# Kernel tuning notes

Hardware: AMD Instinct MI355X
Metric: run time of the kernel (lower is better)

Reference implementation:

```python
import jax, jax.numpy as jnp
import numpy as np

EMBED = 32
HEADS = 8
HEAD_DIM = EMBED // HEADS  # 4


def setup_inputs() -> dict:
    key = jax.random.key(0)
    ks = jax.random.split(key, 12)
    N, Q, K = 4, 2048, 2048
    inp = {
        "query": jax.random.normal(ks[0], (N, Q, EMBED), dtype=jnp.float32),
        "key": jax.random.normal(ks[1], (N, K, EMBED), dtype=jnp.float32),
        "value": jax.random.normal(ks[2], (N, K, EMBED), dtype=jnp.float32),
        "mask": jnp.ones((N, 1, Q, K), dtype=jnp.int32),
        # nn.Linear params: W stored as (in, out) here; math y = x @ W + b
        "Wq": jax.random.normal(ks[3], (EMBED, EMBED), dtype=jnp.float32) / np.sqrt(EMBED),
        "bq": jax.random.normal(ks[4], (EMBED,), dtype=jnp.float32) * 0.01,
        "Wk": jax.random.normal(ks[5], (EMBED, EMBED), dtype=jnp.float32) / np.sqrt(EMBED),
        "bk": jax.random.normal(ks[6], (EMBED,), dtype=jnp.float32) * 0.01,
        "Wv": jax.random.normal(ks[7], (EMBED, EMBED), dtype=jnp.float32) / np.sqrt(EMBED),
        "bv": jax.random.normal(ks[8], (EMBED,), dtype=jnp.float32) * 0.01,
        "Wo": jax.random.normal(ks[9], (EMBED, EMBED), dtype=jnp.float32) / np.sqrt(EMBED),
        "bo": jax.random.normal(ks[10], (EMBED,), dtype=jnp.float32) * 0.01,
    }
    return inp


def reference(query, key, value, mask, Wq, bq, Wk, bk, Wv, bv, Wo, bo):
    N, Qlen, _ = query.shape
    Klen = key.shape[1]
    # linear projections
    q = (query @ Wq + bq).reshape(N, Qlen, HEADS, HEAD_DIM)
    k = (key @ Wk + bk).reshape(N, Klen, HEADS, HEAD_DIM)
    v = (value @ Wv + bv).reshape(N, Klen, HEADS, HEAD_DIM)
    # energy: [N, H, Q, K]
    energy = jnp.einsum("nqhd,nkhd->nhqk", q, k)
    energy = jnp.where(mask == 0, jnp.float32(-1e20), energy)
    # NOTE: original scales by sqrt(embedSize), not sqrt(headDim)
    attn = jax.nn.softmax(energy / jnp.sqrt(jnp.float32(EMBED)), axis=3)
    out = jnp.einsum("nhqv,nvhd->nqhd", attn, v).reshape(N, Qlen, EMBED)
    return out @ Wo + bo
```

## Files before the change

kernel.cpp:

```cpp
#include <hip/hip_runtime.h>

#define NB 4
#define SEQ 2048
#define EMB 32
#define HEADS 8
#define HD 4

typedef float v2f __attribute__((ext_vector_type(2)));
typedef unsigned int uint;

__device__ __forceinline__ v2f splat2(float x) { v2f r; r.x = x; r.y = x; return r; }
__device__ __forceinline__ v2f pkfma(v2f a, v2f b, v2f c) {
  return __builtin_elementwise_fma(a, b, c);
}

__global__ __launch_bounds__(256) void pack_proj_kernel(
    const int* __restrict__ mask, uint* __restrict__ pmw,
    const float* __restrict__ key, const float* __restrict__ value,
    const float* __restrict__ Wk, const float* __restrict__ bk,
    const float* __restrict__ Wv, const float* __restrict__ bv,
    float* __restrict__ Kp, float* __restrict__ Vp) {
  const int packBlocks = NB * SEQ * SEQ / 4 / 256;
  if (blockIdx.x < packBlocks) {
    int g = blockIdx.x * 256 + threadIdx.x;
    const int4 v = ((const int4*)mask)[g];
    uint nib = (uint)(v.x != 0) | ((uint)(v.y != 0) << 1) |
               ((uint)(v.z != 0) << 2) | ((uint)(v.w != 0) << 3);
    int lane = threadIdx.x & 63;
    uint w = nib << (4 * (lane & 7));
    w |= __shfl_xor(w, 1);
    w |= __shfl_xor(w, 2);
    w |= __shfl_xor(w, 4);
    if ((lane & 7) == 0) pmw[g >> 3] = w;
  } else {
    const int half = NB * SEQ / 8;
    int blk2 = blockIdx.x - packBlocks;
    bool isV = blk2 >= half;
    const float* X = isV ? value : key;
    const float* W = isV ? Wv : Wk;
    const float* b = isV ? bv : bk;
    float* P = isV ? Vp : Kp;
    int blk = isV ? (blk2 - half) : blk2;

    __shared__ float sW[EMB][EMB];
    __shared__ float sb[EMB];
    __shared__ float sX[8][EMB];
    int t = threadIdx.x;
    for (int i = t; i < EMB * EMB; i += 256) sW[i >> 5][i & 31] = W[i];
    if (t < EMB) sb[t] = b[t];
    size_t row0 = (size_t)blk * 8;
    int r = t >> 5, c = t & 31;
    sX[r][c] = X[(row0 + r) * EMB + c];
    __syncthreads();
    float acc = sb[c];
#pragma unroll
    for (int d = 0; d < EMB; ++d) acc = fmaf(sX[r][d], sW[d][c], acc);
    P[(row0 + r) * EMB + c] = acc;
  }
}

__device__ __forceinline__ void load_tile(
    const float*& kptr, const float*& vptr,
    float4 (&KK)[4], float4 (&VV)[4]) {
  KK[0] = *(const float4*)(kptr);
  KK[1] = *(const float4*)(kptr + EMB);
  KK[2] = *(const float4*)(kptr + 2 * EMB);
  KK[3] = *(const float4*)(kptr + 3 * EMB);
  VV[0] = *(const float4*)(vptr);
  VV[1] = *(const float4*)(vptr + EMB);
  VV[2] = *(const float4*)(vptr + 2 * EMB);
  VV[3] = *(const float4*)(vptr + 3 * EMB);
  kptr += 32 * EMB; vptr += 32 * EMB;
}

__device__ __forceinline__ void compute_tile(
    const float4 (&KK)[4], const float4 (&VV)[4],
    const v2f (&q2)[4][4], v2f (&l2)[4], v2f (&ac2)[4][4]) {
#pragma unroll
  for (int p = 0; p < 4; ++p) {
    v2f pf[4];
#pragma unroll
    for (int j = 0; j < 4; ++j) {
      const float4 kk = KK[j];
      v2f s = pkfma(q2[p][0], splat2(kk.x),
              pkfma(q2[p][1], splat2(kk.y),
              pkfma(q2[p][2], splat2(kk.z), q2[p][3] * splat2(kk.w))));
      pf[j].x = __builtin_amdgcn_exp2f(s.x);
      pf[j].y = __builtin_amdgcn_exp2f(s.y);
    }
    l2[p] += (pf[0] + pf[1]) + (pf[2] + pf[3]);
#pragma unroll
    for (int j = 0; j < 4; ++j) {
      const float4 vv = VV[j];
      ac2[p][0] = pkfma(pf[j], splat2(vv.x), ac2[p][0]);
      ac2[p][1] = pkfma(pf[j], splat2(vv.y), ac2[p][1]);
      ac2[p][2] = pkfma(pf[j], splat2(vv.z), ac2[p][2]);
      ac2[p][3] = pkfma(pf[j], splat2(vv.w), ac2[p][3]);
    }
  }
}

__device__ __forceinline__ void compute_tile_masked(
    const float4 (&KK)[4], const float4 (&VV)[4],
    const uint (&MW)[8], int ks4,
    const v2f (&q2)[4][4], v2f (&l2)[4], v2f (&ac2)[4][4]) {
#pragma unroll
  for (int p = 0; p < 4; ++p) {
    v2f pf[4];
#pragma unroll
    for (int j = 0; j < 4; ++j) {
      const float4 kk = KK[j];
      v2f s = pkfma(q2[p][0], splat2(kk.x),
              pkfma(q2[p][1], splat2(kk.y),
              pkfma(q2[p][2], splat2(kk.z), q2[p][3] * splat2(kk.w))));
      pf[j].x = ((MW[2 * p + 0] >> (ks4 + j)) & 1u) ? __builtin_amdgcn_exp2f(s.x) : 0.0f;
      pf[j].y = ((MW[2 * p + 1] >> (ks4 + j)) & 1u) ? __builtin_amdgcn_exp2f(s.y) : 0.0f;
    }
    l2[p] += (pf[0] + pf[1]) + (pf[2] + pf[3]);
#pragma unroll
    for (int j = 0; j < 4; ++j) {
      const float4 vv = VV[j];
      ac2[p][0] = pkfma(pf[j], splat2(vv.x), ac2[p][0]);
      ac2[p][1] = pkfma(pf[j], splat2(vv.y), ac2[p][1]);
      ac2[p][2] = pkfma(pf[j], splat2(vv.z), ac2[p][2]);
      ac2[p][3] = pkfma(pf[j], splat2(vv.w), ac2[p][3]);
    }
  }
}

__global__ __launch_bounds__(256, 2) void attn_kernel(
    const float* __restrict__ query, const uint* __restrict__ pmw,
    const float* __restrict__ Kp, const float* __restrict__ Vp,
    const float* __restrict__ Wq, const float* __restrict__ bq,
    const float* __restrict__ Wo, const float* __restrict__ bo,
    float* __restrict__ out) {
  __shared__ float sWq[EMB][EMB];
  __shared__ float sWo[EMB][EMB];
  __shared__ float sbq[EMB];
  __shared__ float sbo[EMB];
  __shared__ float sX[16][EMB];
  __shared__ float sCtx[16][EMB + 1];
  __shared__ float sPart[2][16][EMB];
  __shared__ float sL[2][16][HEADS];

  int t = threadIdx.x;
  int n = blockIdx.x >> 7;
  int qt = blockIdx.x & 127;
  int qrow0 = qt * 16;

  int w = t >> 6;
  int octet = w >> 1;
  int kh = w & 1;
  int lane = t & 63;
  int h = lane & 7;
  int ks = lane >> 3;
  int ks4 = 4 * ks;
  int rbl = 8 * octet;

  for (int i = t; i < EMB * EMB; i += 256) {
    sWq[i >> 5][i & 31] = Wq[i];
    sWo[i >> 5][i & 31] = Wo[i];
  }
  if (t < EMB) { sbq[t] = bq[t]; sbo[t] = bo[t]; }
#pragma unroll
  for (int rr = 0; rr < 2; ++rr) {
    int r = (t >> 5) + 8 * rr, c = t & 31;
    sX[r][c] = query[((size_t)n * SEQ + qrow0 + r) * EMB + c];
  }
  __syncthreads();

  const float SC = 0.17677669529663687f * 1.4426950408889634f;
  v2f q2[4][4];
#pragma unroll
  for (int p = 0; p < 4; ++p)
#pragma unroll
    for (int d = 0; d < 4; ++d) q2[p][d] = splat2(sbq[4 * h + d]);
#pragma unroll
  for (int j = 0; j < EMB; ++j) {
    float w0 = sWq[j][4 * h + 0], w1 = sWq[j][4 * h + 1];
    float w2 = sWq[j][4 * h + 2], w3 = sWq[j][4 * h + 3];
#pragma unroll
    for (int p = 0; p < 4; ++p) {
      v2f x;
      x.x = sX[rbl + 2 * p + 0][j];
      x.y = sX[rbl + 2 * p + 1][j];
      q2[p][0] = pkfma(x, splat2(w0), q2[p][0]);
      q2[p][1] = pkfma(x, splat2(w1), q2[p][1]);
      q2[p][2] = pkfma(x, splat2(w2), q2[p][2]);
      q2[p][3] = pkfma(x, splat2(w3), q2[p][3]);
    }
  }
#pragma unroll
  for (int p = 0; p < 4; ++p)
#pragma unroll
    for (int d = 0; d < 4; ++d) q2[p][d] *= splat2(SC);

  const uint* mbase = pmw + ((size_t)n * SEQ + qrow0 + rbl) * (SEQ / 32) + kh * 32;
  int wl = lane & 7, rl = lane >> 3;
  const uint* mr = mbase + (size_t)rl * 64;
  uint myand = mr[wl] & mr[wl + 8] & mr[wl + 16] & mr[wl + 24];
  bool allones = __all(myand == 0xFFFFFFFFu);

  const float* kptr = Kp + (size_t)n * SEQ * EMB + (size_t)kh * 1024 * EMB
                         + (size_t)ks4 * EMB + 4 * h;
  const float* vptr = Vp + (size_t)n * SEQ * EMB + (size_t)kh * 1024 * EMB
                         + (size_t)ks4 * EMB + 4 * h;

  v2f l2[4], ac2[4][4];
#pragma unroll
  for (int p = 0; p < 4; ++p) {
    l2[p] = splat2(0.0f);
#pragma unroll
    for (int d = 0; d < 4; ++d) ac2[p][d] = splat2(0.0f);
  }

  if (allones) {
    float4 ka[4], va[4], kb[4], vb[4];
    load_tile(kptr, vptr, ka, va);
    for (int i = 0; i < 15; ++i) {
      load_tile(kptr, vptr, kb, vb);
      compute_tile(ka, va, q2, l2, ac2);
      load_tile(kptr, vptr, ka, va);
      compute_tile(kb, vb, q2, l2, ac2);
    }
    load_tile(kptr, vptr, kb, vb);
    compute_tile(ka, va, q2, l2, ac2);
    compute_tile(kb, vb, q2, l2, ac2);
  } else {
    for (int tile = 0; tile < 32; ++tile) {
      float4 ka[4], va[4];
      load_tile(kptr, vptr, ka, va);
      uint MW[8];
#pragma unroll
      for (int rr = 0; rr < 8; ++rr) MW[rr] = mbase[(size_t)rr * 64 + tile];
      compute_tile_masked(ka, va, MW, ks4, q2, l2, ac2);
    }
  }

#pragma unroll
  for (int d = 8; d <= 32; d <<= 1) {
#pragma unroll
    for (int p = 0; p < 4; ++p) {
      l2[p].x += __shfl_xor(l2[p].x, d);
      l2[p].y += __shfl_xor(l2[p].y, d);
#pragma unroll
      for (int e = 0; e < 4; ++e) {
        ac2[p][e].x += __shfl_xor(ac2[p][e].x, d);
        ac2[p][e].y += __shfl_xor(ac2[p][e].y, d);
      }
    }
  }

#pragma unroll
  for (int p = 0; p < 4; ++p) {
    int r0 = rbl + 2 * p;
    if (ks < 4) {
      float vA = (ks == 0) ? ac2[p][0].x : (ks == 1) ? ac2[p][1].x
               : (ks == 2) ? ac2[p][2].x : ac2[p][3].x;
      float vB = (ks == 0) ? ac2[p][0].y : (ks == 1) ? ac2[p][1].y
               : (ks == 2) ? ac2[p][2].y : ac2[p][3].y;
      sPart[kh][r0 + 0][4 * h + ks] = vA;
      sPart[kh][r0 + 1][4 * h + ks] = vB;
    } else if (ks == 4) {
      sL[kh][r0 + 0][h] = l2[p].x;
      sL[kh][r0 + 1][h] = l2[p].y;
    }
  }
  __syncthreads();

#pragma unroll
  for (int rr = 0; rr < 2; ++rr) {
    int r = (t >> 5) + 8 * rr, c = t & 31, hh = (t & 31) >> 2;
    float num = sPart[0][r][c] + sPart[1][r][c];
    float den = sL[0][r][hh] + sL[1][r][hh];
    sCtx[r][c] = num * __builtin_amdgcn_rcpf(den);
  }
  __syncthreads();

#pragma unroll
  for (int rr = 0; rr < 2; ++rr) {
    int r = (t >> 5) + 8 * rr, e = t & 31;
    float o = sbo[e];
#pragma unroll
    for (int j = 0; j < EMB; ++j) o = fmaf(sCtx[r][j], sWo[j][e], o);
    out[((size_t)n * SEQ + qrow0 + r) * EMB + e] = o;
  }
}

extern "C" void kernel_launch(void* const* d_in, const int* in_sizes, int n_in,
                              void* d_out, int out_size, void* d_ws, size_t ws_size,
                              hipStream_t stream) {
  const float* query = (const float*)d_in[0];
  const float* key   = (const float*)d_in[1];
  const float* value = (const float*)d_in[2];
  const int*   mask  = (const int*)d_in[3];
  const float* Wq = (const float*)d_in[4];
  const float* bq = (const float*)d_in[5];
  const float* Wk = (const float*)d_in[6];
  const float* bk = (const float*)d_in[7];
  const float* Wv = (const float*)d_in[8];
  const float* bv = (const float*)d_in[9];
  const float* Wo = (const float*)d_in[10];
  const float* bo = (const float*)d_in[11];
  float* out = (float*)d_out;

  float* Kp = (float*)d_ws;
  float* Vp = Kp + (size_t)NB * SEQ * EMB;
  uint* pmw = (uint*)(Vp + (size_t)NB * SEQ * EMB);

  const int packBlocks = NB * SEQ * SEQ / 4 / 256;
  const int projBlocks = 2 * NB * SEQ / 8;
  pack_proj_kernel<<<dim3(packBlocks + projBlocks), dim3(256), 0, stream>>>(
      mask, pmw, key, value, Wk, bk, Wv, bv, Kp, Vp);
  attn_kernel<<<dim3(NB * (SEQ / 16)), dim3(256), 0, stream>>>(
      query, pmw, Kp, Vp, Wq, bq, Wo, bo, out);
}
```

Measured before the change: 58.98 us.

## Split attention blocks into 8 query rows with four-way key split

The attention kernel now handles 8 query rows per block instead of 16, and its four wavefronts each cover a quarter of the keys (512) instead of two row-groups times two key halves. The grid doubles to 1024 blocks and partial sums are combined across four key quarters in shared memory. This is meant to raise parallelism and shorten each wave's serial loop, at the cost of loading the Wq/Wo weights twice as often across blocks and repeating the Q projection. The launch-bounds occupancy hint is also dropped.

```diff
diff --git a/kernel.cpp b/kernel.cpp
--- a/kernel.cpp
+++ b/kernel.cpp
@@ -128,7 +128,7 @@
   }
 }
 
-__global__ __launch_bounds__(256, 2) void attn_kernel(
+__global__ __launch_bounds__(256) void attn_kernel(
     const float* __restrict__ query, const uint* __restrict__ pmw,
     const float* __restrict__ Kp, const float* __restrict__ Vp,
     const float* __restrict__ Wq, const float* __restrict__ bq,
@@ -138,33 +138,29 @@
   __shared__ float sWo[EMB][EMB];
   __shared__ float sbq[EMB];
   __shared__ float sbo[EMB];
-  __shared__ float sX[16][EMB];
-  __shared__ float sCtx[16][EMB + 1];
-  __shared__ float sPart[2][16][EMB];
-  __shared__ float sL[2][16][HEADS];
+  __shared__ float sX[8][EMB];
+  __shared__ float sCtx[8][EMB + 1];
+  __shared__ float sPart[4][8][EMB];
+  __shared__ float sL[4][8][HEADS];
 
   int t = threadIdx.x;
-  int n = blockIdx.x >> 7;
-  int qt = blockIdx.x & 127;
-  int qrow0 = qt * 16;
-
-  int w = t >> 6;
-  int octet = w >> 1;
-  int kh = w & 1;
+  int n = blockIdx.x >> 8;
+  int qt = blockIdx.x & 255;
+  int qrow0 = qt * 8;
+
+  int kq = t >> 6;
   int lane = t & 63;
   int h = lane & 7;
   int ks = lane >> 3;
   int ks4 = 4 * ks;
-  int rbl = 8 * octet;
 
   for (int i = t; i < EMB * EMB; i += 256) {
     sWq[i >> 5][i & 31] = Wq[i];
     sWo[i >> 5][i & 31] = Wo[i];
   }
   if (t < EMB) { sbq[t] = bq[t]; sbo[t] = bo[t]; }
-#pragma unroll
-  for (int rr = 0; rr < 2; ++rr) {
-    int r = (t >> 5) + 8 * rr, c = t & 31;
+  {
+    int r = t >> 5, c = t & 31;
     sX[r][c] = query[((size_t)n * SEQ + qrow0 + r) * EMB + c];
   }
   __syncthreads();
@@ -177,17 +173,19 @@
     for (int d = 0; d < 4; ++d) q2[p][d] = splat2(sbq[4 * h + d]);
 #pragma unroll
   for (int j = 0; j < EMB; ++j) {
-    float w0 = sWq[j][4 * h + 0], w1 = sWq[j][4 * h + 1];
-    float w2 = sWq[j][4 * h + 2], w3 = sWq[j][4 * h + 3];
+    v2f w0 = splat2(sWq[j][4 * h + 0]);
+    v2f w1 = splat2(sWq[j][4 * h + 1]);
+    v2f w2 = splat2(sWq[j][4 * h + 2]);
+    v2f w3 = splat2(sWq[j][4 * h + 3]);
 #pragma unroll
     for (int p = 0; p < 4; ++p) {
       v2f x;
-      x.x = sX[rbl + 2 * p + 0][j];
-      x.y = sX[rbl + 2 * p + 1][j];
-      q2[p][0] = pkfma(x, splat2(w0), q2[p][0]);
-      q2[p][1] = pkfma(x, splat2(w1), q2[p][1]);
-      q2[p][2] = pkfma(x, splat2(w2), q2[p][2]);
-      q2[p][3] = pkfma(x, splat2(w3), q2[p][3]);
+      x.x = sX[2 * p + 0][j];
+      x.y = sX[2 * p + 1][j];
+      q2[p][0] = pkfma(x, w0, q2[p][0]);
+      q2[p][1] = pkfma(x, w1, q2[p][1]);
+      q2[p][2] = pkfma(x, w2, q2[p][2]);
+      q2[p][3] = pkfma(x, w3, q2[p][3]);
     }
   }
 #pragma unroll
@@ -195,15 +193,15 @@
 #pragma unroll
     for (int d = 0; d < 4; ++d) q2[p][d] *= splat2(SC);
 
-  const uint* mbase = pmw + ((size_t)n * SEQ + qrow0 + rbl) * (SEQ / 32) + kh * 32;
+  const uint* mbase = pmw + ((size_t)n * SEQ + qrow0) * (SEQ / 32) + kq * 16;
   int wl = lane & 7, rl = lane >> 3;
   const uint* mr = mbase + (size_t)rl * 64;
-  uint myand = mr[wl] & mr[wl + 8] & mr[wl + 16] & mr[wl + 24];
+  uint myand = mr[wl] & mr[wl + 8];
   bool allones = __all(myand == 0xFFFFFFFFu);
 
-  const float* kptr = Kp + (size_t)n * SEQ * EMB + (size_t)kh * 1024 * EMB
+  const float* kptr = Kp + (size_t)n * SEQ * EMB + (size_t)kq * 512 * EMB
                          + (size_t)ks4 * EMB + 4 * h;
-  const float* vptr = Vp + (size_t)n * SEQ * EMB + (size_t)kh * 1024 * EMB
+  const float* vptr = Vp + (size_t)n * SEQ * EMB + (size_t)kq * 512 * EMB
                          + (size_t)ks4 * EMB + 4 * h;
 
   v2f l2[4], ac2[4][4];
@@ -217,7 +215,7 @@
   if (allones) {
     float4 ka[4], va[4], kb[4], vb[4];
     load_tile(kptr, vptr, ka, va);
-    for (int i = 0; i < 15; ++i) {
+    for (int i = 0; i < 7; ++i) {
       load_tile(kptr, vptr, kb, vb);
       compute_tile(ka, va, q2, l2, ac2);
       load_tile(kptr, vptr, ka, va);
@@ -227,7 +225,7 @@
     compute_tile(ka, va, q2, l2, ac2);
     compute_tile(kb, vb, q2, l2, ac2);
   } else {
-    for (int tile = 0; tile < 32; ++tile) {
+    for (int tile = 0; tile < 16; ++tile) {
       float4 ka[4], va[4];
       load_tile(kptr, vptr, ka, va);
       uint MW[8];
@@ -253,33 +251,32 @@
 
 #pragma unroll
   for (int p = 0; p < 4; ++p) {
-    int r0 = rbl + 2 * p;
+    int r0 = 2 * p;
     if (ks < 4) {
       float vA = (ks == 0) ? ac2[p][0].x : (ks == 1) ? ac2[p][1].x
                : (ks == 2) ? ac2[p][2].x : ac2[p][3].x;
       float vB = (ks == 0) ? ac2[p][0].y : (ks == 1) ? ac2[p][1].y
                : (ks == 2) ? ac2[p][2].y : ac2[p][3].y;
-      sPart[kh][r0 + 0][4 * h + ks] = vA;
-      sPart[kh][r0 + 1][4 * h + ks] = vB;
+      sPart[kq][r0 + 0][4 * h + ks] = vA;
+      sPart[kq][r0 + 1][4 * h + ks] = vB;
     } else if (ks == 4) {
-      sL[kh][r0 + 0][h] = l2[p].x;
-      sL[kh][r0 + 1][h] = l2[p].y;
+      sL[kq][r0 + 0][h] = l2[p].x;
+      sL[kq][r0 + 1][h] = l2[p].y;
     }
   }
   __syncthreads();
 
-#pragma unroll
-  for (int rr = 0; rr < 2; ++rr) {
-    int r = (t >> 5) + 8 * rr, c = t & 31, hh = (t & 31) >> 2;
-    float num = sPart[0][r][c] + sPart[1][r][c];
-    float den = sL[0][r][hh] + sL[1][r][hh];
+  {
+    int r = t >> 5, c = t & 31, hh = (t & 31) >> 2;
+    float num = (sPart[0][r][c] + sPart[1][r][c]) +
+                (sPart[2][r][c] + sPart[3][r][c]);
+    float den = (sL[0][r][hh] + sL[1][r][hh]) + (sL[2][r][hh] + sL[3][r][hh]);
     sCtx[r][c] = num * __builtin_amdgcn_rcpf(den);
   }
   __syncthreads();
 
-#pragma unroll
-  for (int rr = 0; rr < 2; ++rr) {
-    int r = (t >> 5) + 8 * rr, e = t & 31;
+  {
+    int r = t >> 5, e = t & 31;
     float o = sbo[e];
 #pragma unroll
     for (int j = 0; j < EMB; ++j) o = fmaf(sCtx[r][j], sWo[j][e], o);
@@ -312,6 +309,6 @@
   const int projBlocks = 2 * NB * SEQ / 8;
   pack_proj_kernel<<<dim3(packBlocks + projBlocks), dim3(256), 0, stream>>>(
       mask, pmw, key, value, Wk, bk, Wv, bv, Kp, Vp);
-  attn_kernel<<<dim3(NB * (SEQ / 16)), dim3(256), 0, stream>>>(
+  attn_kernel<<<dim3(NB * (SEQ / 8)), dim3(256), 0, stream>>>(
       query, pmw, Kp, Vp, Wq, bq, Wo, bo, out);
 }
```

New measurement: 65.49 us. 1.11x slower.

## Drop mask bit-packing pass; read int mask directly in attention kernel

Applied to the files above, without the earlier changes.

Removes the separate mask-packing stage and has the attention kernel read the raw int32 mask directly. It checks for an all-ones tile by AND-reducing int4 loads and uses the mask values per element on the masked path. This avoids writing and re-reading a packed bitmask, and the first kernel becomes a pure K/V projection. The inner loops also switch from packed v2f FMAs to scalar FMAs over 8 rows per thread, and the occupancy hint in launch_bounds is removed. The full mask is still read once, now inside attention, and scalar math may issue more instructions than the packed version.

```diff
diff --git a/kernel.cpp b/kernel.cpp
--- a/kernel.cpp
+++ b/kernel.cpp
@@ -6,57 +6,35 @@
 #define HEADS 8
 #define HD 4
 
-typedef float v2f __attribute__((ext_vector_type(2)));
 typedef unsigned int uint;
 
-__device__ __forceinline__ v2f splat2(float x) { v2f r; r.x = x; r.y = x; return r; }
-__device__ __forceinline__ v2f pkfma(v2f a, v2f b, v2f c) {
-  return __builtin_elementwise_fma(a, b, c);
-}
-
-__global__ __launch_bounds__(256) void pack_proj_kernel(
-    const int* __restrict__ mask, uint* __restrict__ pmw,
+__global__ __launch_bounds__(256) void proj_kv_kernel(
     const float* __restrict__ key, const float* __restrict__ value,
     const float* __restrict__ Wk, const float* __restrict__ bk,
     const float* __restrict__ Wv, const float* __restrict__ bv,
     float* __restrict__ Kp, float* __restrict__ Vp) {
-  const int packBlocks = NB * SEQ * SEQ / 4 / 256;
-  if (blockIdx.x < packBlocks) {
-    int g = blockIdx.x * 256 + threadIdx.x;
-    const int4 v = ((const int4*)mask)[g];
-    uint nib = (uint)(v.x != 0) | ((uint)(v.y != 0) << 1) |
-               ((uint)(v.z != 0) << 2) | ((uint)(v.w != 0) << 3);
-    int lane = threadIdx.x & 63;
-    uint w = nib << (4 * (lane & 7));
-    w |= __shfl_xor(w, 1);
-    w |= __shfl_xor(w, 2);
-    w |= __shfl_xor(w, 4);
-    if ((lane & 7) == 0) pmw[g >> 3] = w;
-  } else {
-    const int half = NB * SEQ / 8;
-    int blk2 = blockIdx.x - packBlocks;
-    bool isV = blk2 >= half;
-    const float* X = isV ? value : key;
-    const float* W = isV ? Wv : Wk;
-    const float* b = isV ? bv : bk;
-    float* P = isV ? Vp : Kp;
-    int blk = isV ? (blk2 - half) : blk2;
-
-    __shared__ float sW[EMB][EMB];
-    __shared__ float sb[EMB];
-    __shared__ float sX[8][EMB];
-    int t = threadIdx.x;
-    for (int i = t; i < EMB * EMB; i += 256) sW[i >> 5][i & 31] = W[i];
-    if (t < EMB) sb[t] = b[t];
-    size_t row0 = (size_t)blk * 8;
-    int r = t >> 5, c = t & 31;
-    sX[r][c] = X[(row0 + r) * EMB + c];
-    __syncthreads();
-    float acc = sb[c];
-#pragma unroll
-    for (int d = 0; d < EMB; ++d) acc = fmaf(sX[r][d], sW[d][c], acc);
-    P[(row0 + r) * EMB + c] = acc;
-  }
+  const int half = NB * SEQ / 8;
+  bool isV = blockIdx.x >= half;
+  const float* X = isV ? value : key;
+  const float* W = isV ? Wv : Wk;
+  const float* b = isV ? bv : bk;
+  float* P = isV ? Vp : Kp;
+  int blk = isV ? (blockIdx.x - half) : blockIdx.x;
+
+  __shared__ float sW[EMB][EMB];
+  __shared__ float sb[EMB];
+  __shared__ float sX[8][EMB];
+  int t = threadIdx.x;
+  for (int i = t; i < EMB * EMB; i += 256) sW[i >> 5][i & 31] = W[i];
+  if (t < EMB) sb[t] = b[t];
+  size_t row0 = (size_t)blk * 8;
+  int r = t >> 5, c = t & 31;
+  sX[r][c] = X[(row0 + r) * EMB + c];
+  __syncthreads();
+  float acc = sb[c];
+#pragma unroll
+  for (int d = 0; d < EMB; ++d) acc = fmaf(sX[r][d], sW[d][c], acc);
+  P[(row0 + r) * EMB + c] = acc;
 }
 
 __device__ __forceinline__ void load_tile(
@@ -75,61 +53,49 @@
 
 __device__ __forceinline__ void compute_tile(
     const float4 (&KK)[4], const float4 (&VV)[4],
-    const v2f (&q2)[4][4], v2f (&l2)[4], v2f (&ac2)[4][4]) {
-#pragma unroll
-  for (int p = 0; p < 4; ++p) {
-    v2f pf[4];
-#pragma unroll
-    for (int j = 0; j < 4; ++j) {
-      const float4 kk = KK[j];
-      v2f s = pkfma(q2[p][0], splat2(kk.x),
-              pkfma(q2[p][1], splat2(kk.y),
-              pkfma(q2[p][2], splat2(kk.z), q2[p][3] * splat2(kk.w))));
-      pf[j].x = __builtin_amdgcn_exp2f(s.x);
-      pf[j].y = __builtin_amdgcn_exp2f(s.y);
-    }
-    l2[p] += (pf[0] + pf[1]) + (pf[2] + pf[3]);
-#pragma unroll
-    for (int j = 0; j < 4; ++j) {
-      const float4 vv = VV[j];
-      ac2[p][0] = pkfma(pf[j], splat2(vv.x), ac2[p][0]);
-      ac2[p][1] = pkfma(pf[j], splat2(vv.y), ac2[p][1]);
-      ac2[p][2] = pkfma(pf[j], splat2(vv.z), ac2[p][2]);
-      ac2[p][3] = pkfma(pf[j], splat2(vv.w), ac2[p][3]);
+    const float (&q)[8][4], float (&l)[8], float (&ac)[8][4]) {
+#pragma unroll
+  for (int j = 0; j < 4; ++j) {
+    const float4 kk = KK[j];
+    const float4 vv = VV[j];
+#pragma unroll
+    for (int r = 0; r < 8; ++r) {
+      float s = fmaf(q[r][0], kk.x, fmaf(q[r][1], kk.y,
+                fmaf(q[r][2], kk.z, q[r][3] * kk.w)));
+      float p = __builtin_amdgcn_exp2f(s);
+      l[r] += p;
+      ac[r][0] = fmaf(p, vv.x, ac[r][0]);
+      ac[r][1] = fmaf(p, vv.y, ac[r][1]);
+      ac[r][2] = fmaf(p, vv.z, ac[r][2]);
+      ac[r][3] = fmaf(p, vv.w, ac[r][3]);
     }
   }
 }
 
 __device__ __forceinline__ void compute_tile_masked(
-    const float4 (&KK)[4], const float4 (&VV)[4],
-    const uint (&MW)[8], int ks4,
-    const v2f (&q2)[4][4], v2f (&l2)[4], v2f (&ac2)[4][4]) {
-#pragma unroll
-  for (int p = 0; p < 4; ++p) {
-    v2f pf[4];
-#pragma unroll
-    for (int j = 0; j < 4; ++j) {
-      const float4 kk = KK[j];
-      v2f s = pkfma(q2[p][0], splat2(kk.x),
-              pkfma(q2[p][1], splat2(kk.y),
-              pkfma(q2[p][2], splat2(kk.z), q2[p][3] * splat2(kk.w))));
-      pf[j].x = ((MW[2 * p + 0] >> (ks4 + j)) & 1u) ? __builtin_amdgcn_exp2f(s.x) : 0.0f;
-      pf[j].y = ((MW[2 * p + 1] >> (ks4 + j)) & 1u) ? __builtin_amdgcn_exp2f(s.y) : 0.0f;
-    }
-    l2[p] += (pf[0] + pf[1]) + (pf[2] + pf[3]);
-#pragma unroll
-    for (int j = 0; j < 4; ++j) {
-      const float4 vv = VV[j];
-      ac2[p][0] = pkfma(pf[j], splat2(vv.x), ac2[p][0]);
-      ac2[p][1] = pkfma(pf[j], splat2(vv.y), ac2[p][1]);
-      ac2[p][2] = pkfma(pf[j], splat2(vv.z), ac2[p][2]);
-      ac2[p][3] = pkfma(pf[j], splat2(vv.w), ac2[p][3]);
-    }
-  }
-}
-
-__global__ __launch_bounds__(256, 2) void attn_kernel(
-    const float* __restrict__ query, const uint* __restrict__ pmw,
+    const float4 (&KK)[4], const float4 (&VV)[4], const int4 (&MQ)[8],
+    const float (&q)[8][4], float (&l)[8], float (&ac)[8][4]) {
+#pragma unroll
+  for (int j = 0; j < 4; ++j) {
+    const float4 kk = KK[j];
+    const float4 vv = VV[j];
+#pragma unroll
+    for (int r = 0; r < 8; ++r) {
+      float s = fmaf(q[r][0], kk.x, fmaf(q[r][1], kk.y,
+                fmaf(q[r][2], kk.z, q[r][3] * kk.w)));
+      int m = (j == 0) ? MQ[r].x : (j == 1) ? MQ[r].y : (j == 2) ? MQ[r].z : MQ[r].w;
+      float p = m ? __builtin_amdgcn_exp2f(s) : 0.0f;
+      l[r] += p;
+      ac[r][0] = fmaf(p, vv.x, ac[r][0]);
+      ac[r][1] = fmaf(p, vv.y, ac[r][1]);
+      ac[r][2] = fmaf(p, vv.z, ac[r][2]);
+      ac[r][3] = fmaf(p, vv.w, ac[r][3]);
+    }
+  }
+}
+
+__global__ __launch_bounds__(256) void attn_kernel(
+    const float* __restrict__ query, const int* __restrict__ mask,
     const float* __restrict__ Kp, const float* __restrict__ Vp,
     const float* __restrict__ Wq, const float* __restrict__ bq,
     const float* __restrict__ Wo, const float* __restrict__ bo,
@@ -170,48 +136,53 @@
   __syncthreads();
 
   const float SC = 0.17677669529663687f * 1.4426950408889634f;
-  v2f q2[4][4];
-#pragma unroll
-  for (int p = 0; p < 4; ++p)
-#pragma unroll
-    for (int d = 0; d < 4; ++d) q2[p][d] = splat2(sbq[4 * h + d]);
+  float q[8][4];
+#pragma unroll
+  for (int r = 0; r < 8; ++r)
+#pragma unroll
+    for (int d = 0; d < 4; ++d) q[r][d] = sbq[4 * h + d];
 #pragma unroll
   for (int j = 0; j < EMB; ++j) {
     float w0 = sWq[j][4 * h + 0], w1 = sWq[j][4 * h + 1];
     float w2 = sWq[j][4 * h + 2], w3 = sWq[j][4 * h + 3];
 #pragma unroll
-    for (int p = 0; p < 4; ++p) {
-      v2f x;
-      x.x = sX[rbl + 2 * p + 0][j];
-      x.y = sX[rbl + 2 * p + 1][j];
-      q2[p][0] = pkfma(x, splat2(w0), q2[p][0]);
-      q2[p][1] = pkfma(x, splat2(w1), q2[p][1]);
-      q2[p][2] = pkfma(x, splat2(w2), q2[p][2]);
-      q2[p][3] = pkfma(x, splat2(w3), q2[p][3]);
-    }
-  }
-#pragma unroll
-  for (int p = 0; p < 4; ++p)
-#pragma unroll
-    for (int d = 0; d < 4; ++d) q2[p][d] *= splat2(SC);
-
-  const uint* mbase = pmw + ((size_t)n * SEQ + qrow0 + rbl) * (SEQ / 32) + kh * 32;
-  int wl = lane & 7, rl = lane >> 3;
-  const uint* mr = mbase + (size_t)rl * 64;
-  uint myand = mr[wl] & mr[wl + 8] & mr[wl + 16] & mr[wl + 24];
-  bool allones = __all(myand == 0xFFFFFFFFu);
+    for (int r = 0; r < 8; ++r) {
+      float x = sX[rbl + r][j];
+      q[r][0] = fmaf(x, w0, q[r][0]);
+      q[r][1] = fmaf(x, w1, q[r][1]);
+      q[r][2] = fmaf(x, w2, q[r][2]);
+      q[r][3] = fmaf(x, w3, q[r][3]);
+    }
+  }
+#pragma unroll
+  for (int r = 0; r < 8; ++r)
+#pragma unroll
+    for (int d = 0; d < 4; ++d) q[r][d] *= SC;
+
+  const int* msl = mask + ((size_t)n * SEQ + qrow0 + rbl) * SEQ + kh * 1024;
+  uint andv = 0xFFFFFFFFu;
+#pragma unroll
+  for (int rr = 0; rr < 8; ++rr) {
+    const int4* mrow = (const int4*)(msl + (size_t)rr * SEQ);
+#pragma unroll
+    for (int c = 0; c < 4; ++c) {
+      int4 v = mrow[64 * c + lane];
+      andv &= (uint)v.x & (uint)v.y & (uint)v.z & (uint)v.w;
+    }
+  }
+  bool allones = __all(andv == 0xFFFFFFFFu);
 
   const float* kptr = Kp + (size_t)n * SEQ * EMB + (size_t)kh * 1024 * EMB
                          + (size_t)ks4 * EMB + 4 * h;
   const float* vptr = Vp + (size_t)n * SEQ * EMB + (size_t)kh * 1024 * EMB
                          + (size_t)ks4 * EMB + 4 * h;
 
-  v2f l2[4], ac2[4][4];
-#pragma unroll
-  for (int p = 0; p < 4; ++p) {
-    l2[p] = splat2(0.0f);
-#pragma unroll
-    for (int d = 0; d < 4; ++d) ac2[p][d] = splat2(0.0f);
+  float l[8], ac[8][4];
+#pragma unroll
+  for (int r = 0; r < 8; ++r) {
+    l[r] = 0.0f;
+#pragma unroll
+    for (int d = 0; d < 4; ++d) ac[r][d] = 0.0f;
   }
 
   if (allones) {
@@ -219,52 +190,45 @@
     load_tile(kptr, vptr, ka, va);
     for (int i = 0; i < 15; ++i) {
       load_tile(kptr, vptr, kb, vb);
-      compute_tile(ka, va, q2, l2, ac2);
+      compute_tile(ka, va, q, l, ac);
       load_tile(kptr, vptr, ka, va);
-      compute_tile(kb, vb, q2, l2, ac2);
+      compute_tile(kb, vb, q, l, ac);
     }
     load_tile(kptr, vptr, kb, vb);
-    compute_tile(ka, va, q2, l2, ac2);
-    compute_tile(kb, vb, q2, l2, ac2);
+    compute_tile(ka, va, q, l, ac);
+    compute_tile(kb, vb, q, l, ac);
   } else {
     for (int tile = 0; tile < 32; ++tile) {
       float4 ka[4], va[4];
       load_tile(kptr, vptr, ka, va);
-      uint MW[8];
-#pragma unroll
-      for (int rr = 0; rr < 8; ++rr) MW[rr] = mbase[(size_t)rr * 64 + tile];
-      compute_tile_masked(ka, va, MW, ks4, q2, l2, ac2);
+      int4 MQ[8];
+#pragma unroll
+      for (int rr = 0; rr < 8; ++rr)
+        MQ[rr] = *(const int4*)(msl + (size_t)rr * SEQ + tile * 32 + ks4);
+      compute_tile_masked(ka, va, MQ, q, l, ac);
     }
   }
 
 #pragma unroll
   for (int d = 8; d <= 32; d <<= 1) {
 #pragma unroll
-    for (int p = 0; p < 4; ++p) {
-      l2[p].x += __shfl_xor(l2[p].x, d);
-      l2[p].y += __shfl_xor(l2[p].y, d);
-#pragma unroll
-      for (int e = 0; e < 4; ++e) {
-        ac2[p][e].x += __shfl_xor(ac2[p][e].x, d);
-        ac2[p][e].y += __shfl_xor(ac2[p][e].y, d);
-      }
-    }
-  }
-
-#pragma unroll
-  for (int p = 0; p < 4; ++p) {
-    int r0 = rbl + 2 * p;
-    if (ks < 4) {
-      float vA = (ks == 0) ? ac2[p][0].x : (ks == 1) ? ac2[p][1].x
-               : (ks == 2) ? ac2[p][2].x : ac2[p][3].x;
-      float vB = (ks == 0) ? ac2[p][0].y : (ks == 1) ? ac2[p][1].y
-               : (ks == 2) ? ac2[p][2].y : ac2[p][3].y;
-      sPart[kh][r0 + 0][4 * h + ks] = vA;
-      sPart[kh][r0 + 1][4 * h + ks] = vB;
-    } else if (ks == 4) {
-      sL[kh][r0 + 0][h] = l2[p].x;
-      sL[kh][r0 + 1][h] = l2[p].y;
-    }
+    for (int r = 0; r < 8; ++r) {
+      l[r] += __shfl_xor(l[r], d);
+#pragma unroll
+      for (int e = 0; e < 4; ++e) ac[r][e] += __shfl_xor(ac[r][e], d);
+    }
+  }
+
+  if (ks < 4) {
+#pragma unroll
+    for (int r = 0; r < 8; ++r) {
+      float v = (ks == 0) ? ac[r][0] : (ks == 1) ? ac[r][1]
+              : (ks == 2) ? ac[r][2] : ac[r][3];
+      sPart[kh][rbl + r][4 * h + ks] = v;
+    }
+  } else if (ks == 4) {
+#pragma unroll
+    for (int r = 0; r < 8; ++r) sL[kh][rbl + r][h] = l[r];
   }
   __syncthreads();
 
@@ -306,12 +270,9 @@
 
   float* Kp = (float*)d_ws;
   float* Vp = Kp + (size_t)NB * SEQ * EMB;
-  uint* pmw = (uint*)(Vp + (size_t)NB * SEQ * EMB);
-
-  const int packBlocks = NB * SEQ * SEQ / 4 / 256;
-  const int projBlocks = 2 * NB * SEQ / 8;
-  pack_proj_kernel<<<dim3(packBlocks + projBlocks), dim3(256), 0, stream>>>(
-      mask, pmw, key, value, Wk, bk, Wv, bv, Kp, Vp);
+
+  proj_kv_kernel<<<dim3(2 * NB * SEQ / 8), dim3(256), 0, stream>>>(
+      key, value, Wk, bk, Wv, bv, Kp, Vp);
   attn_kernel<<<dim3(NB * (SEQ / 16)), dim3(256), 0, stream>>>(
-      query, pmw, Kp, Vp, Wq, bq, Wo, bo, out);
-}
+      query, mask, Kp, Vp, Wq, bq, Wo, bo, out);
+}
```

Result: slower. 71.66 us (+21.5%).

## Stage K/V tiles through LDS with async global_load_lds triple buffering

Applied to the files above, without the earlier changes.

In the all-ones mask path, the per-thread global float4 loads of K and V are replaced by a block-wide three-stage LDS ring. Each stage is filled with global_load_lds (16-byte) two tiles ahead, and a waitcnt plus barrier separates the stages. The all-ones mask check is now done once for the whole block through a shared flag rather than per wave. This aims to overlap memory latency with compute and to share K/V loads across the waves that previously fetched overlapping data. In exchange it adds a barrier on every tile and about 48KB of LDS, and drops the occupancy hint of 2 blocks per SM from launch_bounds.

```diff
diff --git a/kernel.cpp b/kernel.cpp
--- a/kernel.cpp
+++ b/kernel.cpp
@@ -12,6 +12,12 @@
 __device__ __forceinline__ v2f splat2(float x) { v2f r; r.x = x; r.y = x; return r; }
 __device__ __forceinline__ v2f pkfma(v2f a, v2f b, v2f c) {
   return __builtin_elementwise_fma(a, b, c);
+}
+
+__device__ __forceinline__ void gll16(const float* src, float* ldsDst) {
+  __builtin_amdgcn_global_load_lds(
+      (const __attribute__((address_space(1))) void*)src,
+      (__attribute__((address_space(3))) void*)ldsDst, 16, 0, 0);
 }
 
 __global__ __launch_bounds__(256) void pack_proj_kernel(
@@ -59,7 +65,62 @@
   }
 }
 
-__device__ __forceinline__ void load_tile(
+__device__ __forceinline__ void compute_math(
+    const float4 (&KK)[4], const float4 (&VV)[4],
+    const v2f (&q2)[4][4], v2f (&l2)[4], v2f (&ac2)[4][4]) {
+#pragma unroll
+  for (int p = 0; p < 4; ++p) {
+    v2f pf[4];
+#pragma unroll
+    for (int j = 0; j < 4; ++j) {
+      const float4 kk = KK[j];
+      v2f s = pkfma(q2[p][0], splat2(kk.x),
+              pkfma(q2[p][1], splat2(kk.y),
+              pkfma(q2[p][2], splat2(kk.z), q2[p][3] * splat2(kk.w))));
+      pf[j].x = __builtin_amdgcn_exp2f(s.x);
+      pf[j].y = __builtin_amdgcn_exp2f(s.y);
+    }
+    l2[p] += (pf[0] + pf[1]) + (pf[2] + pf[3]);
+#pragma unroll
+    for (int j = 0; j < 4; ++j) {
+      const float4 vv = VV[j];
+      ac2[p][0] = pkfma(pf[j], splat2(vv.x), ac2[p][0]);
+      ac2[p][1] = pkfma(pf[j], splat2(vv.y), ac2[p][1]);
+      ac2[p][2] = pkfma(pf[j], splat2(vv.z), ac2[p][2]);
+      ac2[p][3] = pkfma(pf[j], splat2(vv.w), ac2[p][3]);
+    }
+  }
+}
+
+__device__ __forceinline__ void compute_math_masked(
+    const float4 (&KK)[4], const float4 (&VV)[4],
+    const uint (&MW)[8], int ks4,
+    const v2f (&q2)[4][4], v2f (&l2)[4], v2f (&ac2)[4][4]) {
+#pragma unroll
+  for (int p = 0; p < 4; ++p) {
+    v2f pf[4];
+#pragma unroll
+    for (int j = 0; j < 4; ++j) {
+      const float4 kk = KK[j];
+      v2f s = pkfma(q2[p][0], splat2(kk.x),
+              pkfma(q2[p][1], splat2(kk.y),
+              pkfma(q2[p][2], splat2(kk.z), q2[p][3] * splat2(kk.w))));
+      pf[j].x = ((MW[2 * p + 0] >> (ks4 + j)) & 1u) ? __builtin_amdgcn_exp2f(s.x) : 0.0f;
+      pf[j].y = ((MW[2 * p + 1] >> (ks4 + j)) & 1u) ? __builtin_amdgcn_exp2f(s.y) : 0.0f;
+    }
+    l2[p] += (pf[0] + pf[1]) + (pf[2] + pf[3]);
+#pragma unroll
+    for (int j = 0; j < 4; ++j) {
+      const float4 vv = VV[j];
+      ac2[p][0] = pkfma(pf[j], splat2(vv.x), ac2[p][0]);
+      ac2[p][1] = pkfma(pf[j], splat2(vv.y), ac2[p][1]);
+      ac2[p][2] = pkfma(pf[j], splat2(vv.z), ac2[p][2]);
+      ac2[p][3] = pkfma(pf[j], splat2(vv.w), ac2[p][3]);
+    }
+  }
+}
+
+__device__ __forceinline__ void load_tile_g(
     const float*& kptr, const float*& vptr,
     float4 (&KK)[4], float4 (&VV)[4]) {
   KK[0] = *(const float4*)(kptr);
@@ -73,67 +134,14 @@
   kptr += 32 * EMB; vptr += 32 * EMB;
 }
 
-__device__ __forceinline__ void compute_tile(
-    const float4 (&KK)[4], const float4 (&VV)[4],
-    const v2f (&q2)[4][4], v2f (&l2)[4], v2f (&ac2)[4][4]) {
-#pragma unroll
-  for (int p = 0; p < 4; ++p) {
-    v2f pf[4];
-#pragma unroll
-    for (int j = 0; j < 4; ++j) {
-      const float4 kk = KK[j];
-      v2f s = pkfma(q2[p][0], splat2(kk.x),
-              pkfma(q2[p][1], splat2(kk.y),
-              pkfma(q2[p][2], splat2(kk.z), q2[p][3] * splat2(kk.w))));
-      pf[j].x = __builtin_amdgcn_exp2f(s.x);
-      pf[j].y = __builtin_amdgcn_exp2f(s.y);
-    }
-    l2[p] += (pf[0] + pf[1]) + (pf[2] + pf[3]);
-#pragma unroll
-    for (int j = 0; j < 4; ++j) {
-      const float4 vv = VV[j];
-      ac2[p][0] = pkfma(pf[j], splat2(vv.x), ac2[p][0]);
-      ac2[p][1] = pkfma(pf[j], splat2(vv.y), ac2[p][1]);
-      ac2[p][2] = pkfma(pf[j], splat2(vv.z), ac2[p][2]);
-      ac2[p][3] = pkfma(pf[j], splat2(vv.w), ac2[p][3]);
-    }
-  }
-}
-
-__device__ __forceinline__ void compute_tile_masked(
-    const float4 (&KK)[4], const float4 (&VV)[4],
-    const uint (&MW)[8], int ks4,
-    const v2f (&q2)[4][4], v2f (&l2)[4], v2f (&ac2)[4][4]) {
-#pragma unroll
-  for (int p = 0; p < 4; ++p) {
-    v2f pf[4];
-#pragma unroll
-    for (int j = 0; j < 4; ++j) {
-      const float4 kk = KK[j];
-      v2f s = pkfma(q2[p][0], splat2(kk.x),
-              pkfma(q2[p][1], splat2(kk.y),
-              pkfma(q2[p][2], splat2(kk.z), q2[p][3] * splat2(kk.w))));
-      pf[j].x = ((MW[2 * p + 0] >> (ks4 + j)) & 1u) ? __builtin_amdgcn_exp2f(s.x) : 0.0f;
-      pf[j].y = ((MW[2 * p + 1] >> (ks4 + j)) & 1u) ? __builtin_amdgcn_exp2f(s.y) : 0.0f;
-    }
-    l2[p] += (pf[0] + pf[1]) + (pf[2] + pf[3]);
-#pragma unroll
-    for (int j = 0; j < 4; ++j) {
-      const float4 vv = VV[j];
-      ac2[p][0] = pkfma(pf[j], splat2(vv.x), ac2[p][0]);
-      ac2[p][1] = pkfma(pf[j], splat2(vv.y), ac2[p][1]);
-      ac2[p][2] = pkfma(pf[j], splat2(vv.z), ac2[p][2]);
-      ac2[p][3] = pkfma(pf[j], splat2(vv.w), ac2[p][3]);
-    }
-  }
-}
-
-__global__ __launch_bounds__(256, 2) void attn_kernel(
+__global__ __launch_bounds__(256) void attn_kernel(
     const float* __restrict__ query, const uint* __restrict__ pmw,
     const float* __restrict__ Kp, const float* __restrict__ Vp,
     const float* __restrict__ Wq, const float* __restrict__ bq,
     const float* __restrict__ Wo, const float* __restrict__ bo,
     float* __restrict__ out) {
+  __shared__ float sK[3][64][EMB];
+  __shared__ float sV[3][64][EMB];
   __shared__ float sWq[EMB][EMB];
   __shared__ float sWo[EMB][EMB];
   __shared__ float sbq[EMB];
@@ -142,6 +150,7 @@
   __shared__ float sCtx[16][EMB + 1];
   __shared__ float sPart[2][16][EMB];
   __shared__ float sL[2][16][HEADS];
+  __shared__ int sFlag[4];
 
   int t = threadIdx.x;
   int n = blockIdx.x >> 7;
@@ -149,13 +158,32 @@
   int qrow0 = qt * 16;
 
   int w = t >> 6;
-  int octet = w >> 1;
+  int oc = w >> 1;
   int kh = w & 1;
   int lane = t & 63;
   int h = lane & 7;
   int ks = lane >> 3;
   int ks4 = 4 * ks;
-  int rbl = 8 * octet;
+  int h4 = 4 * h;
+  int rbl = 8 * oc;
+
+  const float* Kg = Kp + (size_t)n * SEQ * EMB;
+  const float* Vg = Vp + (size_t)n * SEQ * EMB;
+
+#pragma unroll
+  for (int tt = 0; tt < 2; ++tt) {
+#pragma unroll
+    for (int c = 0; c < 4; ++c) {
+      int idx = w * 4 + c;
+      if (idx < 8) {
+        gll16(Kg + (size_t)tt * 64 * EMB + idx * 256 + lane * 4,
+              &sK[tt][0][0] + idx * 256);
+      } else {
+        gll16(Vg + (size_t)tt * 64 * EMB + (idx - 8) * 256 + lane * 4,
+              &sV[tt][0][0] + (idx - 8) * 256);
+      }
+    }
+  }
 
   for (int i = t; i < EMB * EMB; i += 256) {
     sWq[i >> 5][i & 31] = Wq[i];
@@ -167,44 +195,43 @@
     int r = (t >> 5) + 8 * rr, c = t & 31;
     sX[r][c] = query[((size_t)n * SEQ + qrow0 + r) * EMB + c];
   }
+  {
+    const uint* mb = pmw + ((size_t)n * SEQ + qrow0 + (t >> 4)) * (SEQ / 32);
+    uint4 mw = *(const uint4*)(mb + (t & 15) * 4);
+    uint a = mw.x & mw.y & mw.z & mw.w;
+    bool wall = __all(a == 0xFFFFFFFFu);
+    if (lane == 0) sFlag[w] = wall ? 1 : 0;
+  }
   __syncthreads();
+  bool allones = sFlag[0] && sFlag[1] && sFlag[2] && sFlag[3];
 
   const float SC = 0.17677669529663687f * 1.4426950408889634f;
   v2f q2[4][4];
 #pragma unroll
   for (int p = 0; p < 4; ++p)
 #pragma unroll
-    for (int d = 0; d < 4; ++d) q2[p][d] = splat2(sbq[4 * h + d]);
+    for (int d = 0; d < 4; ++d) q2[p][d] = splat2(sbq[h4 + d]);
 #pragma unroll
   for (int j = 0; j < EMB; ++j) {
-    float w0 = sWq[j][4 * h + 0], w1 = sWq[j][4 * h + 1];
-    float w2 = sWq[j][4 * h + 2], w3 = sWq[j][4 * h + 3];
+    v2f w0 = splat2(sWq[j][h4 + 0]);
+    v2f w1 = splat2(sWq[j][h4 + 1]);
+    v2f w2 = splat2(sWq[j][h4 + 2]);
+    v2f w3 = splat2(sWq[j][h4 + 3]);
 #pragma unroll
     for (int p = 0; p < 4; ++p) {
       v2f x;
       x.x = sX[rbl + 2 * p + 0][j];
       x.y = sX[rbl + 2 * p + 1][j];
-      q2[p][0] = pkfma(x, splat2(w0), q2[p][0]);
-      q2[p][1] = pkfma(x, splat2(w1), q2[p][1]);
-      q2[p][2] = pkfma(x, splat2(w2), q2[p][2]);
-      q2[p][3] = pkfma(x, splat2(w3), q2[p][3]);
+      q2[p][0] = pkfma(x, w0, q2[p][0]);
+      q2[p][1] = pkfma(x, w1, q2[p][1]);
+      q2[p][2] = pkfma(x, w2, q2[p][2]);
+      q2[p][3] = pkfma(x, w3, q2[p][3]);
     }
   }
 #pragma unroll
   for (int p = 0; p < 4; ++p)
 #pragma unroll
     for (int d = 0; d < 4; ++d) q2[p][d] *= splat2(SC);
-
-  const uint* mbase = pmw + ((size_t)n * SEQ + qrow0 + rbl) * (SEQ / 32) + kh * 32;
-  int wl = lane & 7, rl = lane >> 3;
-  const uint* mr = mbase + (size_t)rl * 64;
-  uint myand = mr[wl] & mr[wl + 8] & mr[wl + 16] & mr[wl + 24];
-  bool allones = __all(myand == 0xFFFFFFFFu);
-
-  const float* kptr = Kp + (size_t)n * SEQ * EMB + (size_t)kh * 1024 * EMB
-                         + (size_t)ks4 * EMB + 4 * h;
-  const float* vptr = Vp + (size_t)n * SEQ * EMB + (size_t)kh * 1024 * EMB
-                         + (size_t)ks4 * EMB + 4 * h;
 
   v2f l2[4], ac2[4][4];
 #pragma unroll
@@ -215,25 +242,50 @@
   }
 
   if (allones) {
-    float4 ka[4], va[4], kb[4], vb[4];
-    load_tile(kptr, vptr, ka, va);
-    for (int i = 0; i < 15; ++i) {
-      load_tile(kptr, vptr, kb, vb);
-      compute_tile(ka, va, q2, l2, ac2);
-      load_tile(kptr, vptr, ka, va);
-      compute_tile(kb, vb, q2, l2, ac2);
-    }
-    load_tile(kptr, vptr, kb, vb);
-    compute_tile(ka, va, q2, l2, ac2);
-    compute_tile(kb, vb, q2, l2, ac2);
+    for (int tile = 0; tile < 32; ++tile) {
+      int b = tile % 3;
+      if (tile + 2 < 32) {
+        int b2 = (tile + 2) % 3;
+#pragma unroll
+        for (int c = 0; c < 4; ++c) {
+          int idx = w * 4 + c;
+          if (idx < 8) {
+            gll16(Kg + (size_t)(tile + 2) * 64 * EMB + idx * 256 + lane * 4,
+                  &sK[b2][0][0] + idx * 256);
+          } else {
+            gll16(Vg + (size_t)(tile + 2) * 64 * EMB + (idx - 8) * 256 + lane * 4,
+                  &sV[b2][0][0] + (idx - 8) * 256);
+          }
+        }
+      }
+      {
+        int kb = kh * 32 + ks4;
+        float4 KK[4], VV[4];
+#pragma unroll
+        for (int j = 0; j < 4; ++j) {
+          KK[j] = *(const float4*)(&sK[b][kb + j][h4]);
+          VV[j] = *(const float4*)(&sV[b][kb + j][h4]);
+        }
+        compute_math(KK, VV, q2, l2, ac2);
+      }
+      if (tile + 2 < 32) {
+        asm volatile("s_waitcnt vmcnt(4)" ::: "memory");
+      } else {
+        asm volatile("s_waitcnt vmcnt(0)" ::: "memory");
+      }
+      __builtin_amdgcn_s_barrier();
+    }
   } else {
+    const float* kptr = Kg + (size_t)kh * 1024 * EMB + (size_t)ks4 * EMB + h4;
+    const float* vptr = Vg + (size_t)kh * 1024 * EMB + (size_t)ks4 * EMB + h4;
+    const uint* mbase = pmw + ((size_t)n * SEQ + qrow0 + rbl) * (SEQ / 32) + kh * 32;
     for (int tile = 0; tile < 32; ++tile) {
-      float4 ka[4], va[4];
-      load_tile(kptr, vptr, ka, va);
+      float4 KK[4], VV[4];
+      load_tile_g(kptr, vptr, KK, VV);
       uint MW[8];
 #pragma unroll
       for (int rr = 0; rr < 8; ++rr) MW[rr] = mbase[(size_t)rr * 64 + tile];
-      compute_tile_masked(ka, va, MW, ks4, q2, l2, ac2);
+      compute_math_masked(KK, VV, MW, ks4, q2, l2, ac2);
     }
   }
 
@@ -259,8 +311,8 @@
                : (ks == 2) ? ac2[p][2].x : ac2[p][3].x;
       float vB = (ks == 0) ? ac2[p][0].y : (ks == 1) ? ac2[p][1].y
                : (ks == 2) ? ac2[p][2].y : ac2[p][3].y;
-      sPart[kh][r0 + 0][4 * h + ks] = vA;
-      sPart[kh][r0 + 1][4 * h + ks] = vB;
+      sPart[kh][r0 + 0][h4 + ks] = vA;
+      sPart[kh][r0 + 1][h4 + ks] = vB;
     } else if (ks == 4) {
       sL[kh][r0 + 0][h] = l2[p].x;
       sL[kh][r0 + 1][h] = l2[p].y;
```

Measured after the change: 70.17 us. 1.19x slower.
